# Kernel optimization log

Hardware: AMD Instinct MI355X
Metric: run time of the kernel (lower is better)

## Reference

```python
import jax, jax.numpy as jnp
import numpy as np

GAMMA = 1.0  # matches init_kwargs gamma
B, N, M = 128, 512, 512


def setup_inputs() -> dict:
    key = jax.random.key(0)
    D = jax.random.uniform(key, (B, N, M), dtype=jnp.float32)
    return {"D": D}


def _softmin3(a, b, c, gamma):
    # soft_min over the 3 DP neighbors: -gamma * logsumexp(-x/gamma)
    z = jnp.stack([a, b, c], axis=0) * (-1.0 / gamma)
    return -gamma * jax.nn.logsumexp(z, axis=0)


def reference(D):
    """Soft-DTW forward: returns R[:, N, M], shape (B,).
    DP over rows (lax.scan), inner scan over columns carries R[i, j-1].
    Vectorized over the batch dimension.
    """
    gamma = GAMMA
    b, n, m = D.shape
    dt = D.dtype
    inf = jnp.array(jnp.inf, dt)

    def row_step(prev_row, d_row):
        # prev_row: (b, m+1) = R[i-1, 0..m]; d_row: (b, m) = D[:, i-1, :]
        def col_step(left, xs):
            diag, up, d = xs  # each (b,)
            new = d + _softmin3(diag, up, left, gamma)
            return new, new
        xs = (prev_row[:, :-1].T, prev_row[:, 1:].T, d_row.T)  # each (m, b)
        _, outs = jax.lax.scan(col_step, jnp.full((b,), inf, dt), xs)
        new_row = jnp.concatenate([jnp.full((b, 1), inf, dt), outs.T], axis=1)
        return new_row, None

    # R[0, :] = [0, inf, inf, ...]
    init = jnp.concatenate([jnp.zeros((b, 1), dt), jnp.full((b, m), inf, dt)], axis=1)
    final_row, _ = jax.lax.scan(row_step, init, jnp.swapaxes(D, 0, 1))  # scan over rows (n, b, m)
    return final_row[:, -1]
```

## Files before the change

### kernel.cpp

```cpp
#include <hip/hip_runtime.h>


#define BB 128
#define NN 512
#define MM 512
#define L2E 1.4426950408889634f
#define LN2 0.6931471805599453f

__device__ __forceinline__ int iclamp(int x, int lo, int hi) {
    return x < lo ? lo : (x > hi ? hi : x);
}

template<int PAR, int U>
__device__ __forceinline__ void dostep(
    const float* __restrict__ Db, int k, int jb, int sbase, int tq,
    float (&r1)[8], float (&r2)[8], float4 (&buf)[2][8][2],
    int& irow, float& sh, float& shprev, float& x0)
{
    {
        const int r = iclamp(irow, 0, NN - 1);
        const float4* lp = (const float4*)(Db + ((r << 9) + jb));
        buf[PAR ^ 1][U][0] = lp[0];
        buf[PAR ^ 1][U][1] = lp[1];
        irow += 1;
    }

    float nv[8];
    #pragma unroll
    for (int cc = 7; cc >= 1; --cc) {
        const int c = cc;
        const float up_ = r1[c];
        const float lf  = r1[c - 1];
        const float dg  = r2[c - 1];
        const int par  = (c <= U) ? PAR : (PAR ^ 1);
        const int slot = (c <= U) ? (U - c) : (8 + U - c);
        const float4 f4 = buf[par][slot][c >> 2];
        const float d = ((c & 3) == 0) ? f4.x :
                        ((c & 3) == 1) ? f4.y :
                        ((c & 3) == 2) ? f4.z : f4.w;
        float w = __builtin_amdgcn_exp2f(-L2E * d);
        const bool junk = (sbase + (PAR * 8 + U - c)) >= tq;
        w = junk ? 0.0f : w;
        nv[c] = w * ((up_ + lf) + dg);
    }
    {
        const float up_ = r1[0];
        const float lf  = (k == 0) ? 0.0f : sh;
        const float dg  = (k == 0) ? x0   : shprev;
        const float d   = buf[PAR][U][0].x;
        float w = __builtin_amdgcn_exp2f(-L2E * d);
        const bool junk = (sbase + (PAR * 8 + U)) >= tq;
        w = junk ? 0.0f : w;
        nv[0] = w * ((up_ + lf) + dg);
    }

    x0 = 0.0f;
    #pragma unroll
    for (int c = 0; c < 8; ++c) { r2[c] = r1[c]; r1[c] = nv[c]; }
    shprev = sh;
    sh = __shfl_up(r1[7], 1, 64);
}

__device__ __forceinline__ void renorm(float (&r1)[8], float (&r2)[8],
                                       float& sh, float& shprev, float& gexp)
{
    float mx = r1[0];
    #pragma unroll
    for (int c = 1; c < 8; ++c) mx = __builtin_fmaxf(mx, r1[c]);
    #pragma unroll
    for (int d = 1; d < 64; d <<= 1)
        mx = __builtin_fmaxf(mx, __shfl_xor(mx, d, 64));
    const int eb = (__float_as_int(mx) >> 23) & 255;
    const int ex = (eb > 0 && eb < 255) ? (eb - 127) : 0;
    const float rs = __int_as_float((127 - ex) << 23);
    #pragma unroll
    for (int c = 0; c < 8; ++c) { r1[c] *= rs; r2[c] *= rs; }
    sh *= rs; shprev *= rs;
    gexp += (float)ex;
}

#define STEP8A(DB) \
    dostep<0,0>(DB,k,jb,sbase,tq,r1,r2,buf,irow,sh,shprev,x0); \
    dostep<0,1>(DB,k,jb,sbase,tq,r1,r2,buf,irow,sh,shprev,x0); \
    dostep<0,2>(DB,k,jb,sbase,tq,r1,r2,buf,irow,sh,shprev,x0); \
    dostep<0,3>(DB,k,jb,sbase,tq,r1,r2,buf,irow,sh,shprev,x0); \
    dostep<0,4>(DB,k,jb,sbase,tq,r1,r2,buf,irow,sh,shprev,x0); \
    dostep<0,5>(DB,k,jb,sbase,tq,r1,r2,buf,irow,sh,shprev,x0); \
    dostep<0,6>(DB,k,jb,sbase,tq,r1,r2,buf,irow,sh,shprev,x0); \
    dostep<0,7>(DB,k,jb,sbase,tq,r1,r2,buf,irow,sh,shprev,x0);

#define STEP8B(DB) \
    dostep<1,0>(DB,k,jb,sbase,tq,r1,r2,buf,irow,sh,shprev,x0); \
    dostep<1,1>(DB,k,jb,sbase,tq,r1,r2,buf,irow,sh,shprev,x0); \
    dostep<1,2>(DB,k,jb,sbase,tq,r1,r2,buf,irow,sh,shprev,x0); \
    dostep<1,3>(DB,k,jb,sbase,tq,r1,r2,buf,irow,sh,shprev,x0); \
    dostep<1,4>(DB,k,jb,sbase,tq,r1,r2,buf,irow,sh,shprev,x0); \
    dostep<1,5>(DB,k,jb,sbase,tq,r1,r2,buf,irow,sh,shprev,x0); \
    dostep<1,6>(DB,k,jb,sbase,tq,r1,r2,buf,irow,sh,shprev,x0); \
    dostep<1,7>(DB,k,jb,sbase,tq,r1,r2,buf,irow,sh,shprev,x0);

__launch_bounds__(64, 1)
__global__ void softdtw_wave(const float* __restrict__ D, float* __restrict__ out) {
    const int b = blockIdx.x;
    const int k = threadIdx.x & 63;
    const int jb = k << 3;
    const int tq = jb + NN;
    const float* __restrict__ Db = D + (size_t)b * (NN * MM);

    float r1[8], r2[8];
    float4 buf[2][8][2];
    #pragma unroll
    for (int c = 0; c < 8; ++c) { r1[c] = 0.0f; r2[c] = 0.0f; }
    #pragma unroll
    for (int p = 0; p < 2; ++p)
        #pragma unroll
        for (int w = 0; w < 8; ++w) {
            buf[p][w][0] = make_float4(0.f, 0.f, 0.f, 0.f);
            buf[p][w][1] = make_float4(0.f, 0.f, 0.f, 0.f);
        }

    #pragma unroll
    for (int w = 0; w < 8; ++w) {
        const int i0 = w - jb;
        const int r = iclamp(i0, 0, NN - 1);
        const float4* lp = (const float4*)(Db + ((r << 9) + jb));
        buf[0][w][0] = lp[0];
        buf[0][w][1] = lp[1];
    }

    int irow = 8 - jb;
    float sh = 0.0f, shprev = 0.0f;
    float x0 = 1.0f;
    float gexp = 0.0f;

    #pragma unroll 1
    for (int qq = 0; qq < 63; ++qq) {
        const int sbase = qq << 4;
        renorm(r1, r2, sh, shprev, gexp);
        STEP8A(Db)
        STEP8B(Db)
    }
    {
        const int sbase = 1008;
        renorm(r1, r2, sh, shprev, gexp);
        STEP8A(Db)
        dostep<1,0>(Db,k,jb,sbase,tq,r1,r2,buf,irow,sh,shprev,x0);
        dostep<1,1>(Db,k,jb,sbase,tq,r1,r2,buf,irow,sh,shprev,x0);
        dostep<1,2>(Db,k,jb,sbase,tq,r1,r2,buf,irow,sh,shprev,x0);
        dostep<1,3>(Db,k,jb,sbase,tq,r1,r2,buf,irow,sh,shprev,x0);
        dostep<1,4>(Db,k,jb,sbase,tq,r1,r2,buf,irow,sh,shprev,x0);
        dostep<1,5>(Db,k,jb,sbase,tq,r1,r2,buf,irow,sh,shprev,x0);
        dostep<1,6>(Db,k,jb,sbase,tq,r1,r2,buf,irow,sh,shprev,x0);
    }

    if (k == 63) {
        out[b] = -(__builtin_amdgcn_logf(r1[7]) + gexp) * LN2;
    }
}

extern "C" void kernel_launch(void* const* d_in, const int* in_sizes, int n_in,
                              void* d_out, int out_size, void* d_ws, size_t ws_size,
                              hipStream_t stream) {
    const float* D = (const float*)d_in[0];
    float* out = (float*)d_out;
    softdtw_wave<<<BB, 64, 0, stream>>>(D, out);
}
```

Before: 328.6 us.

## Split each batch's wavefront DP across four waves with LDS boundary exchange

Each batch's anti-diagonal DP moves from one 64-lane wave owning 8 columns per lane to four waves (256 threads) owning 2 columns per lane. Column boundaries between waves pass through shared memory with a workgroup barrier after every step. The max reduction in renormalization now uses DPP row operations plus a cross-wave LDS reduce. The junk-cell masking is skipped in the first half of the iterations. The aim is to cut per-step serial work per lane, at the cost of one block barrier per DP step.

```diff
diff --git a/kernel.cpp b/kernel.cpp
--- a/kernel.cpp
+++ b/kernel.cpp
@@ -11,150 +11,172 @@
     return x < lo ? lo : (x > hi ? hi : x);
 }
 
-template<int PAR, int U>
+template<int CTRL>
+__device__ __forceinline__ float dpp_fmax(float v) {
+    const int s = __builtin_amdgcn_update_dpp(
+        __float_as_int(v), __float_as_int(v), CTRL, 0xF, 0xF, false);
+    return __builtin_fmaxf(v, __int_as_float(s));
+}
+
+template<int P, int U, bool JCHK>
 __device__ __forceinline__ void dostep(
-    const float* __restrict__ Db, int k, int jb, int sbase, int tq,
-    float (&r1)[8], float (&r2)[8], float4 (&buf)[2][8][2],
-    int& irow, float& sh, float& shprev, float& x0)
+    const float* __restrict__ Db, const int lane, const int w,
+    const int jb, const int sbase, const int tq,
+    float (&r1)[2], float (&r2)[2], float2 (&buf)[2][8],
+    int& irow, float& sh, float& shprev, float& bl, float& bd,
+    volatile float (*hs)[2])
 {
     {
         const int r = iclamp(irow, 0, NN - 1);
-        const float4* lp = (const float4*)(Db + ((r << 9) + jb));
-        buf[PAR ^ 1][U][0] = lp[0];
-        buf[PAR ^ 1][U][1] = lp[1];
+        buf[P ^ 1][U] = *(const float2*)(Db + ((r << 9) + jb));
         irow += 1;
     }
 
-    float nv[8];
-    #pragma unroll
-    for (int cc = 7; cc >= 1; --cc) {
-        const int c = cc;
-        const float up_ = r1[c];
-        const float lf  = r1[c - 1];
-        const float dg  = r2[c - 1];
-        const int par  = (c <= U) ? PAR : (PAR ^ 1);
-        const int slot = (c <= U) ? (U - c) : (8 + U - c);
-        const float4 f4 = buf[par][slot][c >> 2];
-        const float d = ((c & 3) == 0) ? f4.x :
-                        ((c & 3) == 1) ? f4.y :
-                        ((c & 3) == 2) ? f4.z : f4.w;
-        float w = __builtin_amdgcn_exp2f(-L2E * d);
-        const bool junk = (sbase + (PAR * 8 + U - c)) >= tq;
-        w = junk ? 0.0f : w;
-        nv[c] = w * ((up_ + lf) + dg);
+    float nv1;
+    {
+        constexpr int par  = (U >= 1) ? P : (P ^ 1);
+        constexpr int slot = (U >= 1) ? (U - 1) : 7;
+        const float d = buf[par][slot].y;
+        float wgt = __builtin_amdgcn_exp2f(-L2E * d);
+        if (JCHK) {
+            const bool junk = (sbase + (P * 8 + U - 1)) >= tq;
+            wgt = junk ? 0.0f : wgt;
+        }
+        nv1 = wgt * ((r1[1] + r1[0]) + r2[0]);
     }
+    if (lane == 63) hs[w][U & 1] = nv1;
+
+    float nv0;
     {
-        const float up_ = r1[0];
-        const float lf  = (k == 0) ? 0.0f : sh;
-        const float dg  = (k == 0) ? x0   : shprev;
-        const float d   = buf[PAR][U][0].x;
-        float w = __builtin_amdgcn_exp2f(-L2E * d);
-        const bool junk = (sbase + (PAR * 8 + U)) >= tq;
-        w = junk ? 0.0f : w;
-        nv[0] = w * ((up_ + lf) + dg);
+        const float lf = (lane == 0) ? bl : sh;
+        const float dg = (lane == 0) ? bd : shprev;
+        const float d  = buf[P][U].x;
+        float wgt = __builtin_amdgcn_exp2f(-L2E * d);
+        if (JCHK) {
+            const bool junk = (sbase + (P * 8 + U)) >= tq;
+            wgt = junk ? 0.0f : wgt;
+        }
+        nv0 = wgt * ((r1[0] + lf) + dg);
     }
 
-    x0 = 0.0f;
-    #pragma unroll
-    for (int c = 0; c < 8; ++c) { r2[c] = r1[c]; r1[c] = nv[c]; }
+    r2[0] = r1[0]; r2[1] = r1[1];
+    r1[0] = nv0;   r1[1] = nv1;
+    bd = bl;
+
+    asm volatile("s_waitcnt lgkmcnt(0)" ::: "memory");
+    __builtin_amdgcn_s_barrier();
+    asm volatile("" ::: "memory");
+
     shprev = sh;
-    sh = __shfl_up(r1[7], 1, 64);
+    sh = __shfl_up(r1[1], 1, 64);
+    if (w > 0) bl = hs[w - 1][U & 1];
 }
 
-__device__ __forceinline__ void renorm(float (&r1)[8], float (&r2)[8],
-                                       float& sh, float& shprev, float& gexp)
+__device__ __forceinline__ void renorm4(
+    const int lane, const int w,
+    float (&r1)[2], float (&r2)[2], float& sh, float& shprev,
+    float& bl, float& bd, float& gexp, volatile float* mxs)
 {
-    float mx = r1[0];
-    #pragma unroll
-    for (int c = 1; c < 8; ++c) mx = __builtin_fmaxf(mx, r1[c]);
-    #pragma unroll
-    for (int d = 1; d < 64; d <<= 1)
-        mx = __builtin_fmaxf(mx, __shfl_xor(mx, d, 64));
-    const int eb = (__float_as_int(mx) >> 23) & 255;
+    float m = __builtin_fmaxf(r1[0], r1[1]);
+    m = dpp_fmax<0x111>(m);
+    m = dpp_fmax<0x112>(m);
+    m = dpp_fmax<0x114>(m);
+    m = dpp_fmax<0x118>(m);
+    m = dpp_fmax<0x142>(m);
+    m = dpp_fmax<0x143>(m);
+    if (lane == 63) mxs[w] = m;
+    asm volatile("s_waitcnt lgkmcnt(0)" ::: "memory");
+    __builtin_amdgcn_s_barrier();
+    asm volatile("" ::: "memory");
+    const float m4 = __builtin_fmaxf(__builtin_fmaxf(mxs[0], mxs[1]),
+                                     __builtin_fmaxf(mxs[2], mxs[3]));
+    const int eb = (__float_as_int(m4) >> 23) & 255;
     const int ex = (eb > 0 && eb < 255) ? (eb - 127) : 0;
     const float rs = __int_as_float((127 - ex) << 23);
-    #pragma unroll
-    for (int c = 0; c < 8; ++c) { r1[c] *= rs; r2[c] *= rs; }
+    r1[0] *= rs; r1[1] *= rs; r2[0] *= rs; r2[1] *= rs;
     sh *= rs; shprev *= rs;
+    bl *= rs;
+    bd *= rs;
     gexp += (float)ex;
 }
 
-#define STEP8A(DB) \
-    dostep<0,0>(DB,k,jb,sbase,tq,r1,r2,buf,irow,sh,shprev,x0); \
-    dostep<0,1>(DB,k,jb,sbase,tq,r1,r2,buf,irow,sh,shprev,x0); \
-    dostep<0,2>(DB,k,jb,sbase,tq,r1,r2,buf,irow,sh,shprev,x0); \
-    dostep<0,3>(DB,k,jb,sbase,tq,r1,r2,buf,irow,sh,shprev,x0); \
-    dostep<0,4>(DB,k,jb,sbase,tq,r1,r2,buf,irow,sh,shprev,x0); \
-    dostep<0,5>(DB,k,jb,sbase,tq,r1,r2,buf,irow,sh,shprev,x0); \
-    dostep<0,6>(DB,k,jb,sbase,tq,r1,r2,buf,irow,sh,shprev,x0); \
-    dostep<0,7>(DB,k,jb,sbase,tq,r1,r2,buf,irow,sh,shprev,x0);
+#define S8(PP, JJ) \
+    dostep<PP,0,JJ>(Db,lane,w,jb,sbase,tq,r1,r2,buf,irow,sh,shprev,bl,bd,hs); \
+    dostep<PP,1,JJ>(Db,lane,w,jb,sbase,tq,r1,r2,buf,irow,sh,shprev,bl,bd,hs); \
+    dostep<PP,2,JJ>(Db,lane,w,jb,sbase,tq,r1,r2,buf,irow,sh,shprev,bl,bd,hs); \
+    dostep<PP,3,JJ>(Db,lane,w,jb,sbase,tq,r1,r2,buf,irow,sh,shprev,bl,bd,hs); \
+    dostep<PP,4,JJ>(Db,lane,w,jb,sbase,tq,r1,r2,buf,irow,sh,shprev,bl,bd,hs); \
+    dostep<PP,5,JJ>(Db,lane,w,jb,sbase,tq,r1,r2,buf,irow,sh,shprev,bl,bd,hs); \
+    dostep<PP,6,JJ>(Db,lane,w,jb,sbase,tq,r1,r2,buf,irow,sh,shprev,bl,bd,hs); \
+    dostep<PP,7,JJ>(Db,lane,w,jb,sbase,tq,r1,r2,buf,irow,sh,shprev,bl,bd,hs);
 
-#define STEP8B(DB) \
-    dostep<1,0>(DB,k,jb,sbase,tq,r1,r2,buf,irow,sh,shprev,x0); \
-    dostep<1,1>(DB,k,jb,sbase,tq,r1,r2,buf,irow,sh,shprev,x0); \
-    dostep<1,2>(DB,k,jb,sbase,tq,r1,r2,buf,irow,sh,shprev,x0); \
-    dostep<1,3>(DB,k,jb,sbase,tq,r1,r2,buf,irow,sh,shprev,x0); \
-    dostep<1,4>(DB,k,jb,sbase,tq,r1,r2,buf,irow,sh,shprev,x0); \
-    dostep<1,5>(DB,k,jb,sbase,tq,r1,r2,buf,irow,sh,shprev,x0); \
-    dostep<1,6>(DB,k,jb,sbase,tq,r1,r2,buf,irow,sh,shprev,x0); \
-    dostep<1,7>(DB,k,jb,sbase,tq,r1,r2,buf,irow,sh,shprev,x0);
-
-__launch_bounds__(64, 1)
-__global__ void softdtw_wave(const float* __restrict__ D, float* __restrict__ out) {
+__launch_bounds__(256, 1)
+__global__ void softdtw_wave4(const float* __restrict__ D, float* __restrict__ out) {
     const int b = blockIdx.x;
-    const int k = threadIdx.x & 63;
-    const int jb = k << 3;
+    const int tid = (int)threadIdx.x;
+    const int w = tid >> 6;
+    const int lane = tid & 63;
+    const int jb = (w << 7) + (lane << 1);
     const int tq = jb + NN;
     const float* __restrict__ Db = D + (size_t)b * (NN * MM);
 
-    float r1[8], r2[8];
-    float4 buf[2][8][2];
+    __shared__ float hsS[4][2];
+    __shared__ float mxsS[4];
+    typedef volatile float vrow_t[2];
+    vrow_t* hs = (vrow_t*)hsS;
+    volatile float* mxs = (volatile float*)mxsS;
+
+    if (tid < 8) ((float*)hsS)[tid] = 0.0f;
+    if (tid < 4) mxsS[tid] = 0.0f;
+    asm volatile("s_waitcnt lgkmcnt(0)" ::: "memory");
+    __builtin_amdgcn_s_barrier();
+    asm volatile("" ::: "memory");
+
+    float r1[2] = {0.0f, 0.0f};
+    float r2[2] = {0.0f, 0.0f};
+    float2 buf[2][8];
     #pragma unroll
-    for (int c = 0; c < 8; ++c) { r1[c] = 0.0f; r2[c] = 0.0f; }
+    for (int v = 0; v < 8; ++v) buf[1][v] = make_float2(0.0f, 0.0f);
     #pragma unroll
-    for (int p = 0; p < 2; ++p)
-        #pragma unroll
-        for (int w = 0; w < 8; ++w) {
-            buf[p][w][0] = make_float4(0.f, 0.f, 0.f, 0.f);
-            buf[p][w][1] = make_float4(0.f, 0.f, 0.f, 0.f);
-        }
-
-    #pragma unroll
-    for (int w = 0; w < 8; ++w) {
-        const int i0 = w - jb;
-        const int r = iclamp(i0, 0, NN - 1);
-        const float4* lp = (const float4*)(Db + ((r << 9) + jb));
-        buf[0][w][0] = lp[0];
-        buf[0][w][1] = lp[1];
+    for (int v = 0; v < 8; ++v) {
+        const int r = iclamp(v - jb, 0, NN - 1);
+        buf[0][v] = *(const float2*)(Db + ((r << 9) + jb));
     }
-
     int irow = 8 - jb;
     float sh = 0.0f, shprev = 0.0f;
-    float x0 = 1.0f;
+    float bl = 0.0f;
+    float bd = (w == 0) ? 1.0f : 0.0f;
     float gexp = 0.0f;
 
     #pragma unroll 1
-    for (int qq = 0; qq < 63; ++qq) {
+    for (int qq = 0; qq < 32; ++qq) {
         const int sbase = qq << 4;
-        renorm(r1, r2, sh, shprev, gexp);
-        STEP8A(Db)
-        STEP8B(Db)
+        renorm4(lane, w, r1, r2, sh, shprev, bl, bd, gexp, mxs);
+        S8(0, false)
+        S8(1, false)
+    }
+    #pragma unroll 1
+    for (int qq = 32; qq < 63; ++qq) {
+        const int sbase = qq << 4;
+        renorm4(lane, w, r1, r2, sh, shprev, bl, bd, gexp, mxs);
+        S8(0, true)
+        S8(1, true)
     }
     {
         const int sbase = 1008;
-        renorm(r1, r2, sh, shprev, gexp);
-        STEP8A(Db)
-        dostep<1,0>(Db,k,jb,sbase,tq,r1,r2,buf,irow,sh,shprev,x0);
-        dostep<1,1>(Db,k,jb,sbase,tq,r1,r2,buf,irow,sh,shprev,x0);
-        dostep<1,2>(Db,k,jb,sbase,tq,r1,r2,buf,irow,sh,shprev,x0);
-        dostep<1,3>(Db,k,jb,sbase,tq,r1,r2,buf,irow,sh,shprev,x0);
-        dostep<1,4>(Db,k,jb,sbase,tq,r1,r2,buf,irow,sh,shprev,x0);
-        dostep<1,5>(Db,k,jb,sbase,tq,r1,r2,buf,irow,sh,shprev,x0);
-        dostep<1,6>(Db,k,jb,sbase,tq,r1,r2,buf,irow,sh,shprev,x0);
+        renorm4(lane, w, r1, r2, sh, shprev, bl, bd, gexp, mxs);
+        S8(0, true)
+        dostep<1,0,true>(Db,lane,w,jb,sbase,tq,r1,r2,buf,irow,sh,shprev,bl,bd,hs);
+        dostep<1,1,true>(Db,lane,w,jb,sbase,tq,r1,r2,buf,irow,sh,shprev,bl,bd,hs);
+        dostep<1,2,true>(Db,lane,w,jb,sbase,tq,r1,r2,buf,irow,sh,shprev,bl,bd,hs);
+        dostep<1,3,true>(Db,lane,w,jb,sbase,tq,r1,r2,buf,irow,sh,shprev,bl,bd,hs);
+        dostep<1,4,true>(Db,lane,w,jb,sbase,tq,r1,r2,buf,irow,sh,shprev,bl,bd,hs);
+        dostep<1,5,true>(Db,lane,w,jb,sbase,tq,r1,r2,buf,irow,sh,shprev,bl,bd,hs);
+        dostep<1,6,true>(Db,lane,w,jb,sbase,tq,r1,r2,buf,irow,sh,shprev,bl,bd,hs);
     }
 
-    if (k == 63) {
-        out[b] = -(__builtin_amdgcn_logf(r1[7]) + gexp) * LN2;
+    if (w == 3 && lane == 63) {
+        out[b] = -(__builtin_amdgcn_logf(r1[1]) + gexp) * LN2;
     }
 }
 
@@ -163,5 +185,5 @@
                               hipStream_t stream) {
     const float* D = (const float*)d_in[0];
     float* out = (float*)d_out;
-    softdtw_wave<<<BB, 64, 0, stream>>>(D, out);
+    softdtw_wave4<<<BB, 256, 0, stream>>>(D, out);
 }
```

Measured after the change: 697.7 us. 112% more time.
